# Optimization experiments

Measured on AMD Instinct MI355X. Metric: run time of the kernel, lower is better.

## Reference

```python
import jax, jax.numpy as jnp
import numpy as np
import math

EMBED = 1024
HEADS = 16
HEAD_DIM = EMBED // HEADS


def setup_inputs() -> dict:
    key = jax.random.key(0)
    ks = jax.random.split(key, 6)
    scale = 1.0 / math.sqrt(EMBED)
    x = jax.random.normal(ks[0], (4, 2048, EMBED), dtype=jnp.float32)
    Wv = jax.random.normal(ks[1], (EMBED, EMBED), dtype=jnp.float32) * scale
    Wk = jax.random.normal(ks[2], (EMBED, EMBED), dtype=jnp.float32) * scale
    Wq = jax.random.normal(ks[3], (EMBED, EMBED), dtype=jnp.float32) * scale
    Wo = jax.random.normal(ks[4], (EMBED, EMBED), dtype=jnp.float32) * scale
    bo = jax.random.normal(ks[5], (EMBED,), dtype=jnp.float32) * 0.02
    return {"x": x, "Wq": Wq, "Wk": Wk, "Wv": Wv, "Wo": Wo, "bo": bo}


def reference(x, Wq, Wk, Wv, Wo, bo):
    N, S, E = x.shape
    H, D = HEADS, HEAD_DIM
    # Linear(E,E,bias=False): y = x @ W.T ; weights here stored as [out,in]
    q = (x @ Wq.T).reshape(N, S, H, D)
    k = (x @ Wk.T).reshape(N, S, H, D)
    v = (x @ Wv.T).reshape(N, S, H, D)
    energy = jnp.einsum('nqhd,nkhd->nhqk', q, k)  # [N,H,S,S]
    attn = jax.nn.softmax(energy / math.sqrt(D), axis=-1)
    out = jnp.einsum('nhql,nlhd->nqhd', attn, v).reshape(N, S, E)
    return out @ Wo.T + bo
```

## Files before the change

### kernel.cpp

```cpp
#include <hip/hip_runtime.h>
#include <stdint.h>

#define NB   4
#define SLEN 2048
#define EMB  1024
#define NH   16
#define HD   64
#define MTOT (NB * SLEN)

typedef __bf16 bf8_t  __attribute__((ext_vector_type(8)));
typedef __bf16 bf4_t  __attribute__((ext_vector_type(4)));
typedef float  f4_t   __attribute__((ext_vector_type(4)));
typedef unsigned int u32x2 __attribute__((ext_vector_type(2)));
typedef unsigned int u32x4 __attribute__((ext_vector_type(4)));

#if __has_builtin(__builtin_amdgcn_exp2f)
#define EXP2(x) __builtin_amdgcn_exp2f(x)
#else
#define EXP2(x) exp2f(x)
#endif

__device__ __forceinline__ void gld16(const void* g, void* l) {
    __builtin_amdgcn_global_load_lds(
        (__attribute__((address_space(1))) void*)(g),
        (__attribute__((address_space(3))) void*)(l),
        16, 0, 0);
}

__device__ __forceinline__ uint32_t pack_bf16_rtn(float a, float b) {
    uint32_t ua = __builtin_bit_cast(uint32_t, a) + 0x8000u;
    uint32_t ub = __builtin_bit_cast(uint32_t, b) + 0x8000u;
    return __builtin_amdgcn_perm(ub, ua, 0x07060302u);
}
__device__ __forceinline__ uint32_t pack_bf16_rtz(float a, float b) {
    return __builtin_amdgcn_perm(__builtin_bit_cast(uint32_t, b),
                                 __builtin_bit_cast(uint32_t, a), 0x07060302u);
}

__global__ __launch_bounds__(256) void cast_all(const float* __restrict__ x,
                                                const float* __restrict__ Wq,
                                                const float* __restrict__ Wk,
                                                const float* __restrict__ Wv,
                                                const float* __restrict__ Wo,
                                                __bf16* __restrict__ xb,
                                                __bf16* __restrict__ wb) {
    int b = blockIdx.x;
    const float* s;
    __bf16* d;
    float sc = 1.0f;
    if (b < 8192) {
        s = x; d = xb;
    } else {
        int y = (b - 8192) >> 10;
        s = (y == 0) ? Wq : (y == 1) ? Wk : (y == 2) ? Wv : Wo;
        d = wb + (size_t)y * (EMB * EMB);
        b = (b - 8192) & 1023;
        if (y == 0) sc = 0.125f * 1.44269504f;
    }
    int i = (b * 256 + (int)threadIdx.x) * 4;
    float4 f = *(const float4*)(s + i);
    bf4_t o = { (__bf16)(f.x * sc), (__bf16)(f.y * sc),
                (__bf16)(f.z * sc), (__bf16)(f.w * sc) };
    *(bf4_t*)(d + i) = o;
}

__device__ __forceinline__ void gstage(const __bf16* __restrict__ A,
                                       const __bf16* __restrict__ B,
                                       int m0, int n0, int k0, int K, int tid,
                                       __bf16* __restrict__ As,
                                       __bf16* __restrict__ Bs) {
#pragma unroll
    for (int t = 0; t < 4; ++t) {
        int c   = t * 256 + tid;
        int row = c >> 3;
        int kc  = (c & 7) ^ (row & 7);
        int cb  = c & ~63;
        gld16(A + (size_t)(m0 + row) * K + k0 + kc * 8, As + cb * 8);
        gld16(B + (size_t)(n0 + row) * K + k0 + kc * 8, Bs + cb * 8);
    }
}

template <bool SWAP>
__device__ __forceinline__ void gcompute(const __bf16* __restrict__ As,
                                         const __bf16* __restrict__ Bs,
                                         f4_t (*acc)[4],
                                         int wm, int wn, int quad, int l16) {
#pragma unroll
    for (int ks = 0; ks < 2; ++ks) {
        bf8_t af[4], bfr[4];
#pragma unroll
        for (int i = 0; i < 4; ++i) {
            int r = wm + i * 16 + l16;
            af[i] = *(const bf8_t*)&As[r * 64 + (((ks * 4 + quad) ^ (r & 7)) * 8)];
        }
#pragma unroll
        for (int j = 0; j < 4; ++j) {
            int r = wn + j * 16 + l16;
            bfr[j] = *(const bf8_t*)&Bs[r * 64 + (((ks * 4 + quad) ^ (r & 7)) * 8)];
        }
#pragma unroll
        for (int i = 0; i < 4; ++i)
#pragma unroll
            for (int j = 0; j < 4; ++j) {
                if (SWAP)
                    acc[i][j] = __builtin_amdgcn_mfma_f32_16x16x32_bf16(
                        bfr[j], af[i], acc[i][j], 0, 0, 0);
                else
                    acc[i][j] = __builtin_amdgcn_mfma_f32_16x16x32_bf16(
                        af[i], bfr[j], acc[i][j], 0, 0, 0);
            }
    }
}

template <bool SWAP>
__device__ __forceinline__ void gkloop(const __bf16* __restrict__ A,
                                       const __bf16* __restrict__ B,
                                       int m0, int n0, int K, int tid,
                                       __bf16* As0, __bf16* Bs0,
                                       __bf16* As1, __bf16* Bs1,
                                       f4_t (*acc)[4],
                                       int wm, int wn, int quad, int l16) {
    gstage(A, B, m0, n0, 0, K, tid, As0, Bs0);
    int k0 = 0;
    for (; k0 + 128 < K; k0 += 128) {
        __syncthreads();
        gstage(A, B, m0, n0, k0 + 64, K, tid, As1, Bs1);
        gcompute<SWAP>(As0, Bs0, acc, wm, wn, quad, l16);
        __syncthreads();
        gstage(A, B, m0, n0, k0 + 128, K, tid, As0, Bs0);
        gcompute<SWAP>(As1, Bs1, acc, wm, wn, quad, l16);
    }
    __syncthreads();
    gstage(A, B, m0, n0, k0 + 64, K, tid, As1, Bs1);
    gcompute<SWAP>(As0, Bs0, acc, wm, wn, quad, l16);
    __syncthreads();
    gcompute<SWAP>(As1, Bs1, acc, wm, wn, quad, l16);
}

__global__ __launch_bounds__(256, 2) void proj_qkv(const __bf16* __restrict__ A,
                                                   const __bf16* __restrict__ B,
                                                   __bf16* __restrict__ qb) {
    __shared__ __bf16 As0[128 * 64], Bs0[128 * 64];
    __shared__ __bf16 As1[128 * 64], Bs1[128 * 64];

    const int tid  = threadIdx.x;
    const int lane = tid & 63;
    const int w    = tid >> 6;
    const int quad = lane >> 4;
    const int l16  = lane & 15;
    const int m0   = blockIdx.x * 128;
    const int n0   = blockIdx.y * 128;
    const int wm   = (w >> 1) * 64;
    const int wn   = (w & 1) * 64;

    f4_t acc[4][4];
#pragma unroll
    for (int i = 0; i < 4; ++i)
#pragma unroll
        for (int j = 0; j < 4; ++j) acc[i][j] = (f4_t){0.f, 0.f, 0.f, 0.f};

    if (n0 < 2048) {
        gkloop<true>(A, B, m0, n0, EMB, tid, As0, Bs0, As1, Bs1, acc, wm, wn, quad, l16);
#pragma unroll
        for (int i = 0; i < 4; ++i)
#pragma unroll
            for (int j = 0; j < 4; ++j) {
                int m   = m0 + wm + i * 16 + l16;
                int col = n0 + wn + j * 16 + quad * 4;
                __bf16* dst = (col < 1024) ? qb : qb + (size_t)8 * 1024 * 1024;
                bf4_t pk = { (__bf16)acc[i][j][0], (__bf16)acc[i][j][1],
                             (__bf16)acc[i][j][2], (__bf16)acc[i][j][3] };
                *(bf4_t*)&dst[(size_t)m * 1024 + (col & 1023)] = pk;
            }
    } else {
        gkloop<false>(A, B, m0, n0, EMB, tid, As0, Bs0, As1, Bs1, acc, wm, wn, quad, l16);
        __bf16* vtb = qb + (size_t)16 * 1024 * 1024;
#pragma unroll
        for (int i = 0; i < 4; ++i)
#pragma unroll
            for (int j = 0; j < 4; ++j) {
                int m  = m0 + wm + i * 16 + quad * 4;
                int ch = n0 - 2048 + wn + j * 16 + l16;
                size_t idx = ((size_t)(m >> 11) * 1024 + ch) * 2048 + (m & 2047);
                bf4_t pk = { (__bf16)acc[i][j][0], (__bf16)acc[i][j][1],
                             (__bf16)acc[i][j][2], (__bf16)acc[i][j][3] };
                *(bf4_t*)&vtb[idx] = pk;
            }
    }
}

__global__ __launch_bounds__(256, 2) void gemm_out(const __bf16* __restrict__ A,
                                                   const __bf16* __restrict__ B,
                                                   float* __restrict__ C,
                                                   const float* __restrict__ bias) {
    __shared__ __bf16 As0[128 * 64], Bs0[128 * 64];
    __shared__ __bf16 As1[128 * 64], Bs1[128 * 64];

    const int tid  = threadIdx.x;
    const int lane = tid & 63;
    const int w    = tid >> 6;
    const int quad = lane >> 4;
    const int l16  = lane & 15;
    const int m0   = blockIdx.x * 128;
    const int n0   = blockIdx.y * 128;
    const int wm   = (w >> 1) * 64;
    const int wn   = (w & 1) * 64;

    f4_t acc[4][4];
#pragma unroll
    for (int i = 0; i < 4; ++i)
#pragma unroll
        for (int j = 0; j < 4; ++j) acc[i][j] = (f4_t){0.f, 0.f, 0.f, 0.f};

    gkloop<true>(A, B, m0, n0, EMB, tid, As0, Bs0, As1, Bs1, acc, wm, wn, quad, l16);

#pragma unroll
    for (int i = 0; i < 4; ++i)
#pragma unroll
        for (int j = 0; j < 4; ++j) {
            int m   = m0 + wm + i * 16 + l16;
            int col = n0 + wn + j * 16 + quad * 4;
            float4 bv = *(const float4*)&bias[col];
            float4 ov = { acc[i][j][0] + bv.x, acc[i][j][1] + bv.y,
                          acc[i][j][2] + bv.z, acc[i][j][3] + bv.w };
            *(float4*)&C[(size_t)m * EMB + col] = ov;
        }
}

__device__ __forceinline__ void attn_stage(const __bf16* __restrict__ kbase,
                                           const __bf16* __restrict__ vbase,
                                           int l0, int tid,
                                           __bf16* __restrict__ Ksb,
                                           __bf16* __restrict__ Vsb) {
    int c   = tid;
    int row = c >> 3;
    int kc  = (c & 7) ^ (row & 7);
    int cb  = c & ~63;
    gld16(kbase + (size_t)(l0 + row) * EMB + kc * 8, Ksb + cb * 8);
    gld16(vbase + (size_t)row * SLEN + l0 + kc * 8, Vsb + cb * 8);
}

__device__ __forceinline__ void qkexp_half(const __bf16* __restrict__ Ksb, int ks,
                                           const bf8_t (*bq)[2],
                                           uint32_t (*pk)[4],
                                           int quad, int l16, int sw) {
#pragma unroll
    for (int jkl = 0; jkl < 2; ++jkl) {
        const int jk = ks * 2 + jkl;
        bf8_t ak0 = *(const bf8_t*)&Ksb[(jk * 16 + l16) * 64 + ((quad ^ sw) * 8)];
        bf8_t ak1 = *(const bf8_t*)&Ksb[(jk * 16 + l16) * 64 + (((4 + quad) ^ sw) * 8)];
#pragma unroll
        for (int jq = 0; jq < 2; ++jq) {
            f4_t e = (f4_t){0.f, 0.f, 0.f, 0.f};
            e = __builtin_amdgcn_mfma_f32_16x16x32_bf16(ak0, bq[jq][0], e, 0, 0, 0);
            e = __builtin_amdgcn_mfma_f32_16x16x32_bf16(ak1, bq[jq][1], e, 0, 0, 0);
            pk[jq][jkl * 2 + 0] = pack_bf16_rtz(EXP2(e[0]), EXP2(e[1]));
            pk[jq][jkl * 2 + 1] = pack_bf16_rtz(EXP2(e[2]), EXP2(e[3]));
        }
    }
}

__device__ __forceinline__ void pv_half(const __bf16* __restrict__ Vsb, int ks,
                                        const uint32_t (*pk)[4], bf8_t aones,
                                        f4_t* ls, f4_t (*o)[4],
                                        int quad, int l16, int sw) {
    bf8_t bp[2];
#pragma unroll
    for (int jq = 0; jq < 2; ++jq) {
        u32x2 s0 = __builtin_amdgcn_permlane32_swap(pk[jq][0], pk[jq][2], false, false);
        u32x2 s1 = __builtin_amdgcn_permlane32_swap(pk[jq][1], pk[jq][3], false, false);
        u32x2 t0 = __builtin_amdgcn_permlane16_swap(s0[0], s0[1], false, false);
        u32x2 t1 = __builtin_amdgcn_permlane16_swap(s1[0], s1[1], false, false);
        bp[jq] = __builtin_bit_cast(bf8_t, (u32x4){t0[0], t1[0], t0[1], t1[1]});
    }
    __builtin_amdgcn_s_setprio(1);
#pragma unroll
    for (int jq = 0; jq < 2; ++jq)
        ls[jq] = __builtin_amdgcn_mfma_f32_16x16x32_bf16(aones, bp[jq], ls[jq], 0, 0, 0);
#pragma unroll
    for (int jd = 0; jd < 4; ++jd) {
        bf8_t av = *(const bf8_t*)&Vsb[(jd * 16 + l16) * 64 +
                                       (((ks * 4 + quad) ^ sw) * 8)];
#pragma unroll
        for (int jq = 0; jq < 2; ++jq)
            o[jq][jd] = __builtin_amdgcn_mfma_f32_16x16x32_bf16(av, bp[jq],
                                                                o[jq][jd], 0, 0, 0);
    }
    __builtin_amdgcn_s_setprio(0);
}

__device__ __forceinline__ void attn_pair(const __bf16* __restrict__ Ka,
                                          const __bf16* __restrict__ Kb,
                                          const __bf16* __restrict__ Va,
                                          const __bf16* __restrict__ Vb,
                                          const bf8_t (*bq)[2], bf8_t aones,
                                          f4_t* ls, f4_t (*o)[4],
                                          int quad, int l16, int sw) {
    uint32_t pkA[2][4], pkB[2][4];
    qkexp_half(Ka, 0, bq, pkA, quad, l16, sw);
    qkexp_half(Ka, 1, bq, pkB, quad, l16, sw);
    pv_half(Va, 0, pkA, aones, ls, o, quad, l16, sw);
    qkexp_half(Kb, 0, bq, pkA, quad, l16, sw);
    pv_half(Va, 1, pkB, aones, ls, o, quad, l16, sw);
    qkexp_half(Kb, 1, bq, pkB, quad, l16, sw);
    pv_half(Vb, 0, pkA, aones, ls, o, quad, l16, sw);
    pv_half(Vb, 1, pkB, aones, ls, o, quad, l16, sw);
}

__global__ __launch_bounds__(512, 4) void attn_fwd(const __bf16* __restrict__ Q,
                                                   const __bf16* __restrict__ K,
                                                   const __bf16* __restrict__ Vt,
                                                   __bf16* __restrict__ O) {
    __shared__ __bf16 Ks0[64 * 64], Ks1[64 * 64];
    __shared__ __bf16 Ks2[64 * 64], Ks3[64 * 64];
    __shared__ __bf16 Vs0[64 * 64], Vs1[64 * 64];
    __shared__ __bf16 Vs2[64 * 64], Vs3[64 * 64];

    const int tid  = threadIdx.x;
    const int lane = tid & 63;
    const int w    = tid >> 6;
    const int quad = lane >> 4;
    const int l16  = lane & 15;
    const int nh   = blockIdx.x;
    const int n    = nh >> 4;
    const int h    = nh & 15;
    const int q0   = blockIdx.y * 256 + w * 32;

    bf8_t bq[2][2];
#pragma unroll
    for (int jq = 0; jq < 2; ++jq)
#pragma unroll
        for (int ks = 0; ks < 2; ++ks)
            bq[jq][ks] = *(const bf8_t*)(Q + (size_t)(n * SLEN + q0 + jq * 16 + l16) * EMB +
                                         h * HD + ks * 32 + quad * 8);

    bf8_t aones;
#pragma unroll
    for (int t = 0; t < 8; ++t) aones[t] = (__bf16)1.0f;

    f4_t ls[2];
    f4_t o[2][4];
#pragma unroll
    for (int jq = 0; jq < 2; ++jq) {
        ls[jq] = (f4_t){0.f, 0.f, 0.f, 0.f};
#pragma unroll
        for (int jd = 0; jd < 4; ++jd) o[jq][jd] = (f4_t){0.f, 0.f, 0.f, 0.f};
    }

    const __bf16* kbase = K + (size_t)n * SLEN * EMB + h * HD;
    const __bf16* vbase = Vt + (size_t)nh * HD * SLEN;
    const int sw = l16 & 7;

    attn_stage(kbase, vbase, 0, tid, Ks0, Vs0);
    attn_stage(kbase, vbase, 64, tid, Ks1, Vs1);

    int it = 0;
    for (; it < 14; it += 2) {
        int L = it * 128;
        __syncthreads();
        attn_stage(kbase, vbase, L + 128, tid, Ks2, Vs2);
        attn_stage(kbase, vbase, L + 192, tid, Ks3, Vs3);
        attn_pair(Ks0, Ks1, Vs0, Vs1, bq, aones, ls, o, quad, l16, sw);
        __syncthreads();
        attn_stage(kbase, vbase, L + 256, tid, Ks0, Vs0);
        attn_stage(kbase, vbase, L + 320, tid, Ks1, Vs1);
        attn_pair(Ks2, Ks3, Vs2, Vs3, bq, aones, ls, o, quad, l16, sw);
    }
    {
        int L = it * 128;
        __syncthreads();
        attn_stage(kbase, vbase, L + 128, tid, Ks2, Vs2);
        attn_stage(kbase, vbase, L + 192, tid, Ks3, Vs3);
        attn_pair(Ks0, Ks1, Vs0, Vs1, bq, aones, ls, o, quad, l16, sw);
        __syncthreads();
        attn_pair(Ks2, Ks3, Vs2, Vs3, bq, aones, ls, o, quad, l16, sw);
    }

#pragma unroll
    for (int jq = 0; jq < 2; ++jq) {
        float inv = 1.0f / ls[jq][0];
#pragma unroll
        for (int jd = 0; jd < 4; ++jd) {
            uint32_t d0 = pack_bf16_rtn(o[jq][jd][0] * inv, o[jq][jd][1] * inv);
            uint32_t d1 = pack_bf16_rtn(o[jq][jd][2] * inv, o[jq][jd][3] * inv);
            *(uint2*)&O[(size_t)(n * SLEN + q0 + jq * 16 + l16) * EMB + h * HD +
                        jd * 16 + quad * 4] = (uint2){d0, d1};
        }
    }
}

extern "C" void kernel_launch(void* const* d_in, const int* in_sizes, int n_in,
                              void* d_out, int out_size, void* d_ws, size_t ws_size,
                              hipStream_t stream) {
    const float* x  = (const float*)d_in[0];
    const float* Wq = (const float*)d_in[1];
    const float* Wk = (const float*)d_in[2];
    const float* Wv = (const float*)d_in[3];
    const float* Wo = (const float*)d_in[4];
    const float* bo = (const float*)d_in[5];

    char* wsb = (char*)d_ws;
    const size_t MB = (size_t)1 << 20;
    __bf16* xb  = (__bf16*)(wsb + 0 * MB);
    __bf16* ab  = xb;
    __bf16* wqb = (__bf16*)(wsb + 16 * MB);
    __bf16* wob = (__bf16*)(wsb + 22 * MB);
    __bf16* qb  = (__bf16*)(wsb + 24 * MB);
    __bf16* kb  = (__bf16*)(wsb + 40 * MB);
    __bf16* vtb = (__bf16*)(wsb + 56 * MB);

    cast_all<<<dim3(12288), dim3(256), 0, stream>>>(x, Wq, Wk, Wv, Wo, xb, wqb);

    proj_qkv<<<dim3(MTOT / 128, 3072 / 128), 256, 0, stream>>>(xb, wqb, qb);

    attn_fwd<<<dim3(NB * NH, SLEN / 256), 512, 0, stream>>>(qb, kb, vtb, ab);

    gemm_out<<<dim3(MTOT / 128, EMB / 128), 256, 0, stream>>>(ab, wob, (float*)d_out, bo);
}
```

Before: 240.2 us.

## Load V fragments directly from global and remap GEMM blocks by XCD

The attention kernel stops staging V tiles in LDS. Each lane now reads its V fragments straight from global memory (L2/cache) into registers, which halves LDS use and the async copy traffic per iteration but exposes global-load latency inside the PV loop. Both GEMM kernels switch to a 1D grid with a swizzle that assigns contiguous tile ranges to each of the 8 XCDs, to improve L2 reuse of A/B panels.

```diff
diff --git a/kernel.cpp b/kernel.cpp
--- a/kernel.cpp
+++ b/kernel.cpp
@@ -148,8 +148,10 @@
     const int w    = tid >> 6;
     const int quad = lane >> 4;
     const int l16  = lane & 15;
-    const int m0   = blockIdx.x * 128;
-    const int n0   = blockIdx.y * 128;
+    const int lin  = blockIdx.x;
+    const int sl   = (lin & 7) * 192 + (lin >> 3);
+    const int m0   = (sl & 63) * 128;
+    const int n0   = (sl >> 6) * 128;
     const int wm   = (w >> 1) * 64;
     const int wn   = (w & 1) * 64;
 
@@ -201,8 +203,10 @@
     const int w    = tid >> 6;
     const int quad = lane >> 4;
     const int l16  = lane & 15;
-    const int m0   = blockIdx.x * 128;
-    const int n0   = blockIdx.y * 128;
+    const int lin  = blockIdx.x;
+    const int sl   = (lin & 7) * 64 + (lin >> 3);
+    const int m0   = (sl & 63) * 128;
+    const int n0   = (sl >> 6) * 128;
     const int wm   = (w >> 1) * 64;
     const int wn   = (w & 1) * 64;
 
@@ -228,16 +232,13 @@
 }
 
 __device__ __forceinline__ void attn_stage(const __bf16* __restrict__ kbase,
-                                           const __bf16* __restrict__ vbase,
                                            int l0, int tid,
-                                           __bf16* __restrict__ Ksb,
-                                           __bf16* __restrict__ Vsb) {
+                                           __bf16* __restrict__ Ksb) {
     int c   = tid;
     int row = c >> 3;
     int kc  = (c & 7) ^ (row & 7);
     int cb  = c & ~63;
     gld16(kbase + (size_t)(l0 + row) * EMB + kc * 8, Ksb + cb * 8);
-    gld16(vbase + (size_t)row * SLEN + l0 + kc * 8, Vsb + cb * 8);
 }
 
 __device__ __forceinline__ void qkexp_half(const __bf16* __restrict__ Ksb, int ks,
@@ -260,10 +261,13 @@
     }
 }
 
-__device__ __forceinline__ void pv_half(const __bf16* __restrict__ Vsb, int ks,
+__device__ __forceinline__ void pv_half(const __bf16* __restrict__ vpl0, int ks,
                                         const uint32_t (*pk)[4], bf8_t aones,
-                                        f4_t* ls, f4_t (*o)[4],
-                                        int quad, int l16, int sw) {
+                                        f4_t* ls, f4_t (*o)[4]) {
+    bf8_t av[4];
+#pragma unroll
+    for (int jd = 0; jd < 4; ++jd)
+        av[jd] = *(const bf8_t*)(vpl0 + ks * 32 + (size_t)jd * 16 * SLEN);
     bf8_t bp[2];
 #pragma unroll
     for (int jq = 0; jq < 2; ++jq) {
@@ -278,33 +282,29 @@
     for (int jq = 0; jq < 2; ++jq)
         ls[jq] = __builtin_amdgcn_mfma_f32_16x16x32_bf16(aones, bp[jq], ls[jq], 0, 0, 0);
 #pragma unroll
-    for (int jd = 0; jd < 4; ++jd) {
-        bf8_t av = *(const bf8_t*)&Vsb[(jd * 16 + l16) * 64 +
-                                       (((ks * 4 + quad) ^ sw) * 8)];
+    for (int jd = 0; jd < 4; ++jd)
 #pragma unroll
         for (int jq = 0; jq < 2; ++jq)
-            o[jq][jd] = __builtin_amdgcn_mfma_f32_16x16x32_bf16(av, bp[jq],
+            o[jq][jd] = __builtin_amdgcn_mfma_f32_16x16x32_bf16(av[jd], bp[jq],
                                                                 o[jq][jd], 0, 0, 0);
-    }
     __builtin_amdgcn_s_setprio(0);
 }
 
 __device__ __forceinline__ void attn_pair(const __bf16* __restrict__ Ka,
                                           const __bf16* __restrict__ Kb,
-                                          const __bf16* __restrict__ Va,
-                                          const __bf16* __restrict__ Vb,
+                                          const __bf16* __restrict__ vgl, int L,
                                           const bf8_t (*bq)[2], bf8_t aones,
                                           f4_t* ls, f4_t (*o)[4],
                                           int quad, int l16, int sw) {
     uint32_t pkA[2][4], pkB[2][4];
     qkexp_half(Ka, 0, bq, pkA, quad, l16, sw);
     qkexp_half(Ka, 1, bq, pkB, quad, l16, sw);
-    pv_half(Va, 0, pkA, aones, ls, o, quad, l16, sw);
+    pv_half(vgl + L, 0, pkA, aones, ls, o);
     qkexp_half(Kb, 0, bq, pkA, quad, l16, sw);
-    pv_half(Va, 1, pkB, aones, ls, o, quad, l16, sw);
+    pv_half(vgl + L, 1, pkB, aones, ls, o);
     qkexp_half(Kb, 1, bq, pkB, quad, l16, sw);
-    pv_half(Vb, 0, pkA, aones, ls, o, quad, l16, sw);
-    pv_half(Vb, 1, pkB, aones, ls, o, quad, l16, sw);
+    pv_half(vgl + L + 64, 0, pkA, aones, ls, o);
+    pv_half(vgl + L + 64, 1, pkB, aones, ls, o);
 }
 
 __global__ __launch_bounds__(512, 4) void attn_fwd(const __bf16* __restrict__ Q,
@@ -313,8 +313,6 @@
                                                    __bf16* __restrict__ O) {
     __shared__ __bf16 Ks0[64 * 64], Ks1[64 * 64];
     __shared__ __bf16 Ks2[64 * 64], Ks3[64 * 64];
-    __shared__ __bf16 Vs0[64 * 64], Vs1[64 * 64];
-    __shared__ __bf16 Vs2[64 * 64], Vs3[64 * 64];
 
     const int tid  = threadIdx.x;
     const int lane = tid & 63;
@@ -347,33 +345,33 @@
         for (int jd = 0; jd < 4; ++jd) o[jq][jd] = (f4_t){0.f, 0.f, 0.f, 0.f};
     }
 
-    const __bf16* kbase = K + (size_t)n * SLEN * EMB + h * HD;
-    const __bf16* vbase = Vt + (size_t)nh * HD * SLEN;
+    const __bf16* kbase  = K + (size_t)n * SLEN * EMB + h * HD;
+    const __bf16* vglane = Vt + (size_t)nh * HD * SLEN + (size_t)l16 * SLEN + quad * 8;
     const int sw = l16 & 7;
 
-    attn_stage(kbase, vbase, 0, tid, Ks0, Vs0);
-    attn_stage(kbase, vbase, 64, tid, Ks1, Vs1);
+    attn_stage(kbase, 0, tid, Ks0);
+    attn_stage(kbase, 64, tid, Ks1);
 
     int it = 0;
     for (; it < 14; it += 2) {
         int L = it * 128;
         __syncthreads();
-        attn_stage(kbase, vbase, L + 128, tid, Ks2, Vs2);
-        attn_stage(kbase, vbase, L + 192, tid, Ks3, Vs3);
-        attn_pair(Ks0, Ks1, Vs0, Vs1, bq, aones, ls, o, quad, l16, sw);
-        __syncthreads();
-        attn_stage(kbase, vbase, L + 256, tid, Ks0, Vs0);
-        attn_stage(kbase, vbase, L + 320, tid, Ks1, Vs1);
-        attn_pair(Ks2, Ks3, Vs2, Vs3, bq, aones, ls, o, quad, l16, sw);
+        attn_stage(kbase, L + 128, tid, Ks2);
+        attn_stage(kbase, L + 192, tid, Ks3);
+        attn_pair(Ks0, Ks1, vglane, L, bq, aones, ls, o, quad, l16, sw);
+        __syncthreads();
+        attn_stage(kbase, L + 256, tid, Ks0);
+        attn_stage(kbase, L + 320, tid, Ks1);
+        attn_pair(Ks2, Ks3, vglane, L + 128, bq, aones, ls, o, quad, l16, sw);
     }
     {
         int L = it * 128;
         __syncthreads();
-        attn_stage(kbase, vbase, L + 128, tid, Ks2, Vs2);
-        attn_stage(kbase, vbase, L + 192, tid, Ks3, Vs3);
-        attn_pair(Ks0, Ks1, Vs0, Vs1, bq, aones, ls, o, quad, l16, sw);
-        __syncthreads();
-        attn_pair(Ks2, Ks3, Vs2, Vs3, bq, aones, ls, o, quad, l16, sw);
+        attn_stage(kbase, L + 128, tid, Ks2);
+        attn_stage(kbase, L + 192, tid, Ks3);
+        attn_pair(Ks0, Ks1, vglane, L, bq, aones, ls, o, quad, l16, sw);
+        __syncthreads();
+        attn_pair(Ks2, Ks3, vglane, L + 128, bq, aones, ls, o, quad, l16, sw);
     }
 
 #pragma unroll
@@ -411,9 +409,9 @@
 
     cast_all<<<dim3(12288), dim3(256), 0, stream>>>(x, Wq, Wk, Wv, Wo, xb, wqb);
 
-    proj_qkv<<<dim3(MTOT / 128, 3072 / 128), 256, 0, stream>>>(xb, wqb, qb);
+    proj_qkv<<<dim3(1536), 256, 0, stream>>>(xb, wqb, qb);
 
     attn_fwd<<<dim3(NB * NH, SLEN / 256), 512, 0, stream>>>(qb, kb, vtb, ab);
 
-    gemm_out<<<dim3(MTOT / 128, EMB / 128), 256, 0, stream>>>(ab, wob, (float*)d_out, bo);
-}
+    gemm_out<<<dim3(512), 256, 0, stream>>>(ab, wob, (float*)d_out, bo);
+}
```

Result: slower. 319.5 us (+33.0%).
